# Performance work log

Hardware: AMD Instinct MI355X
Metric: run time of the kernel (lower is better)

The kernel has to match this reference:

```python
import jax, jax.numpy as jnp
import numpy as np

T, B, H, L = 512, 64, 512, 2  # seq len, batch, hidden (=input_size), num_layers


def setup_inputs() -> dict:
    key = jax.random.key(0)
    ks = jax.random.split(key, 8)
    s = 1.0 / np.sqrt(H)  # PyTorch LSTMCell init scale
    return {
        "x": jax.random.normal(ks[0], (T, B, H), dtype=jnp.float32),
        "hx": jax.random.normal(ks[1], (L, B, H), dtype=jnp.float32),
        "cx": jax.random.normal(ks[2], (L, B, H), dtype=jnp.float32),
        "W_ih": jax.random.uniform(ks[3], (L, 4 * H, H), jnp.float32, -s, s),
        "W_hh": jax.random.uniform(ks[4], (L, 4 * H, H), jnp.float32, -s, s),
        "b_ih": jax.random.uniform(ks[5], (L, 4 * H), jnp.float32, -s, s),
        "b_hh": jax.random.uniform(ks[6], (L, 4 * H), jnp.float32, -s, s),
    }


def _lstm_cell(x, h, c, W_ih, W_hh, b_ih, b_hh):
    # gates: [B, 4H], PyTorch gate order i, f, g, o
    gates = x @ W_ih.T + b_ih + h @ W_hh.T + b_hh
    i, f, g, o = jnp.split(gates, 4, axis=-1)
    c_new = jax.nn.sigmoid(f) * c + jax.nn.sigmoid(i) * jnp.tanh(g)
    h_new = jax.nn.sigmoid(o) * jnp.tanh(c_new)
    return h_new, c_new


def reference(x, hx, cx, W_ih, W_hh, b_ih, b_hh):
    num_layers = W_ih.shape[0]

    def step(carry, x_t):
        hs, cs = carry  # each [L, B, H]
        inp = x_t
        new_h, new_c = [], []
        for l in range(num_layers):
            h, c = _lstm_cell(inp, hs[l], cs[l], W_ih[l], W_hh[l], b_ih[l], b_hh[l])
            new_h.append(h)
            new_c.append(c)
            inp = h  # feed current-timestep output to next layer (matches torch code)
        return (jnp.stack(new_h), jnp.stack(new_c)), inp

    (hx_f, cx_f), output = jax.lax.scan(step, (hx, cx), x)
    return output, (hx_f, cx_f)
```

## Files before the change

kernel.cpp:

```cpp
#include <hip/hip_runtime.h>
#include <hip/hip_bf16.h>
#include <stdint.h>

#define Tn 512
#define Bn 64
#define Hn 512
#define LDP 520
#define NWG 128
#define NTHR 512
#define BnHn (Bn * Hn)

typedef unsigned short u16;
typedef unsigned int u32;
typedef unsigned long long u64;
typedef __attribute__((ext_vector_type(8))) short bf16x8;
typedef __attribute__((ext_vector_type(4))) float f32x4;

#define GO_OFF   2048
#define HIST_OFF 16384

__device__ __forceinline__ u16 f2bf(float f) {
  u32 u = __float_as_uint(f);
  u = (u + 0x7FFFu + ((u >> 16) & 1u)) >> 16;
  return (u16)u;
}
__device__ __forceinline__ float sigf(float x) { return 1.f / (1.f + __expf(-x)); }
__device__ __forceinline__ float mytanh(float x) {
  float e = __expf(2.f * x);
  return 1.f - 2.f / (e + 1.f);
}

extern "C" __global__ void __launch_bounds__(256)
lstm_prep(const float* __restrict__ x, const float* __restrict__ hx,
          u32* __restrict__ ws, int xok, int histok) {
  u16* hist = (u16*)((char*)ws + HIST_OFF);
  u16* xbf  = hist + (size_t)(histok ? 513 : 2) * 2 * BnHn;
  const int slot_init = histok ? 512 : 1;
  const int gt = blockIdx.x * 256 + threadIdx.x;
  if (xok) {
#pragma unroll
    for (int i = 0; i < 8; ++i) {
      const int c = gt + (i << 19);
      const float4 v = *(const float4*)(x + (size_t)c * 4);
      const u64 pk = (u64)((u32)f2bf(v.x) | ((u32)f2bf(v.y) << 16)) |
                     ((u64)((u32)f2bf(v.z) | ((u32)f2bf(v.w) << 16)) << 32);
      *(u64*)(xbf + (size_t)c * 4) = pk;
    }
  }
  if (gt < 32768) {
    const int e0 = 2 * gt;
    const int l = e0 >> 15;
    const int off = e0 & 32767;
    const u32 pk = (u32)f2bf(hx[e0]) | ((u32)f2bf(hx[e0 + 1]) << 16);
    *(u32*)(hist + ((size_t)slot_init * 2 + l) * BnHn + off) = pk;
  }
}

extern "C" __global__ void __launch_bounds__(NTHR, 2)
lstm_fused(const float* __restrict__ x, const float* __restrict__ hx,
           const float* __restrict__ cx, const float* __restrict__ Wih,
           const float* __restrict__ Whh, const float* __restrict__ bih,
           const float* __restrict__ bhh, float* __restrict__ out,
           u32* __restrict__ ws, int xok, int histok) {
  __shared__ u16 sh_inp[32 * LDP];
  __shared__ u16 sh_h[32 * LDP];
  __shared__ u32 sh_flag;

  __builtin_amdgcn_fence(__ATOMIC_ACQUIRE, "agent");

  const int wg = blockIdx.x;
  const int tid = threadIdx.x;
  const int layer = wg >> 6;
  const int rem = wg & 63;
  const int shalf = rem >> 5;
  const int cc = rem & 31;
  const int wave = tid >> 6;
  const int lane = tid & 63;
  const int l15 = lane & 15;
  const int lhi = lane >> 4;
  const int mt = wave >> 1;
  const int nt = wave & 1;
  const bool leader_wg = (layer == 0) && (cc == 0);

  u32* slots = ws;
  u32* gof   = ws + GO_OFF;
  u16* hist  = (u16*)((char*)ws + HIST_OFF);
  u16* xbf   = hist + (size_t)(histok ? 513 : 2) * 2 * BnHn;

  if (tid == 0) sh_flag = 0;

  const int jrow = mt * 16 + l15;
  const int gateA = jrow & 3, colA = jrow >> 2;
  const int growA = gateA * Hn + cc * 16 + colA;
  const float* wihp = Wih + ((size_t)layer * 4 * Hn + growA) * Hn;
  const float* whhp = Whh + ((size_t)layer * 4 * Hn + growA) * Hn;
  bf16x8 wih_f[16], whh_f[16];
#pragma unroll
  for (int kt = 0; kt < 16; ++kt) {
    const int k0 = kt * 32 + lhi * 8;
    const float4 va0 = *(const float4*)(wihp + k0);
    const float4 va1 = *(const float4*)(wihp + k0 + 4);
    const float4 vb0 = *(const float4*)(whhp + k0);
    const float4 vb1 = *(const float4*)(whhp + k0 + 4);
    bf16x8 a, b;
    a[0]=(short)f2bf(va0.x); a[1]=(short)f2bf(va0.y); a[2]=(short)f2bf(va0.z); a[3]=(short)f2bf(va0.w);
    a[4]=(short)f2bf(va1.x); a[5]=(short)f2bf(va1.y); a[6]=(short)f2bf(va1.z); a[7]=(short)f2bf(va1.w);
    b[0]=(short)f2bf(vb0.x); b[1]=(short)f2bf(vb0.y); b[2]=(short)f2bf(vb0.z); b[3]=(short)f2bf(vb0.w);
    b[4]=(short)f2bf(vb1.x); b[5]=(short)f2bf(vb1.y); b[6]=(short)f2bf(vb1.z); b[7]=(short)f2bf(vb1.w);
    wih_f[kt] = a; whh_f[kt] = b;
  }

  const int colE = cc * 16 + mt * 4 + lhi;
  const int sampE = shalf * 32 + nt * 16 + l15;
  float bias[4];
#pragma unroll
  for (int r = 0; r < 4; ++r) {
    const int grow = r * Hn + cc * 16 + mt * 4 + lhi;
    bias[r] = bih[layer * 4 * Hn + grow] + bhh[layer * 4 * Hn + grow];
  }
  float c_cur = cx[((size_t)layer * Bn + sampE) * Hn + colE];

  auto stage_x = [&](int t) {
    if (xok) {
      const u16* ip = xbf + ((size_t)t * Bn + shalf * 32) * Hn;
#pragma unroll
      for (int i = 0; i < 4; ++i) {
        const int chunk = tid + i * 512;
        const int row = chunk >> 6, c0 = (chunk & 63) * 8;
        const uint4 v = *(const uint4*)(ip + (size_t)row * Hn + c0);
        *(uint4*)(&sh_inp[row * LDP + c0]) = v;
      }
    } else {
      const float* xp = x + ((size_t)t * Bn + shalf * 32) * Hn;
#pragma unroll
      for (int i = 0; i < 8; ++i) {
        const int chunk = tid + i * 512;
        const int row = chunk >> 7, c0 = (chunk & 127) * 4;
        const float4 v = *(const float4*)(xp + (size_t)row * Hn + c0);
        const u32 p0 = (u32)f2bf(v.x) | ((u32)f2bf(v.y) << 16);
        const u32 p1 = (u32)f2bf(v.z) | ((u32)f2bf(v.w) << 16);
        *(uint2*)(&sh_inp[row * LDP + c0]) = make_uint2(p0, p1);
      }
    }
  };
  if (layer == 0) stage_x(0);

  u32 ep = 0;
  for (int s = 0; s <= Tn; ++s) {
    const int t = layer ? s - 1 : s;
    const bool act = (t >= 0) && (t < Tn);

    if (act) {
      const int slotR = histok ? ((t == 0) ? 512 : (t - 1)) : ((t - 1) & 1);
      const u16* hp = hist + ((size_t)slotR * 2 + layer) * BnHn + (size_t)(shalf * 32) * Hn;
      if (histok) {
#pragma unroll
        for (int i = 0; i < 4; ++i) {
          const int chunk = tid + i * 512;
          const int row = chunk >> 6, c0 = (chunk & 63) * 8;
          const uint4 v = *(const uint4*)(hp + (size_t)row * Hn + c0);
          *(uint4*)(&sh_h[row * LDP + c0]) = v;
        }
      } else {
#pragma unroll
        for (int i = 0; i < 8; ++i) {
          const int chunk = tid + i * 512;
          const int row = chunk >> 7, c0 = (chunk & 127) * 4;
          const u64 v = __hip_atomic_load((const u64*)(hp + (size_t)row * Hn + c0),
                                          __ATOMIC_RELAXED, __HIP_MEMORY_SCOPE_AGENT);
          *(u64*)(&sh_h[row * LDP + c0]) = v;
        }
      }
      if (layer == 1) {
        const int slotI = histok ? t : (t & 1);
        const u16* ip = hist + ((size_t)slotI * 2 + 0) * BnHn + (size_t)(shalf * 32) * Hn;
        if (histok) {
#pragma unroll
          for (int i = 0; i < 4; ++i) {
            const int chunk = tid + i * 512;
            const int row = chunk >> 6, c0 = (chunk & 63) * 8;
            const uint4 v = *(const uint4*)(ip + (size_t)row * Hn + c0);
            *(uint4*)(&sh_inp[row * LDP + c0]) = v;
          }
        } else {
#pragma unroll
          for (int i = 0; i < 8; ++i) {
            const int chunk = tid + i * 512;
            const int row = chunk >> 7, c0 = (chunk & 127) * 4;
            const u64 v = __hip_atomic_load((const u64*)(ip + (size_t)row * Hn + c0),
                                            __ATOMIC_RELAXED, __HIP_MEMORY_SCOPE_AGENT);
            *(u64*)(&sh_inp[row * LDP + c0]) = v;
          }
        }
      }
    }
    __syncthreads();

    float hn = 0.f, cn = 0.f;
    if (act) {
      f32x4 a0 = {0,0,0,0}, a1 = {0,0,0,0}, b0 = {0,0,0,0}, b1 = {0,0,0,0};
      const int brow = (nt * 16 + l15) * LDP;
#pragma unroll
      for (int kt = 0; kt < 16; kt += 2) {
        const bf16x8 bi0 = *(const bf16x8*)(&sh_inp[brow + kt * 32 + lhi * 8]);
        const bf16x8 bh0 = *(const bf16x8*)(&sh_h[brow + kt * 32 + lhi * 8]);
        const bf16x8 bi1 = *(const bf16x8*)(&sh_inp[brow + (kt + 1) * 32 + lhi * 8]);
        const bf16x8 bh1 = *(const bf16x8*)(&sh_h[brow + (kt + 1) * 32 + lhi * 8]);
        a0 = __builtin_amdgcn_mfma_f32_16x16x32_bf16(wih_f[kt], bi0, a0, 0, 0, 0);
        b0 = __builtin_amdgcn_mfma_f32_16x16x32_bf16(whh_f[kt], bh0, b0, 0, 0, 0);
        a1 = __builtin_amdgcn_mfma_f32_16x16x32_bf16(wih_f[kt + 1], bi1, a1, 0, 0, 0);
        b1 = __builtin_amdgcn_mfma_f32_16x16x32_bf16(whh_f[kt + 1], bh1, b1, 0, 0, 0);
      }
      const float gi = a0[0] + a1[0] + b0[0] + b1[0] + bias[0];
      const float gf = a0[1] + a1[1] + b0[1] + b1[1] + bias[1];
      const float gg = a0[2] + a1[2] + b0[2] + b1[2] + bias[2];
      const float go_ = a0[3] + a1[3] + b0[3] + b1[3] + bias[3];
      cn = sigf(gf) * c_cur + sigf(gi) * mytanh(gg);
      hn = sigf(go_) * mytanh(cn);
      c_cur = cn;

      const u32 hu = (u32)f2bf(hn);
      const u32 pair = hu | (__shfl_xor(hu, 16) << 16);
      const u32 hi2 = __shfl_xor(pair, 32);
      if (lhi == 0) {
        const int slotW = histok ? t : (t & 1);
        const u64 v8 = (u64)pair | ((u64)hi2 << 32);
        u16* wp = hist + ((size_t)slotW * 2 + layer) * BnHn + (size_t)sampE * Hn + cc * 16 + mt * 4;
        __hip_atomic_store((u64*)wp, v8, __ATOMIC_RELAXED, __HIP_MEMORY_SCOPE_AGENT);
      }
    }
    asm volatile("s_waitcnt vmcnt(0)" ::: "memory");
    __syncthreads();
    ++ep;
    if (tid == 0)
      __hip_atomic_store(&slots[wg * 16], ep, __ATOMIC_RELAXED, __HIP_MEMORY_SCOPE_AGENT);

    if (act) {
      if (layer == 1)
        out[((size_t)t * Bn + sampE) * Hn + colE] = hn;
      if (t == Tn - 1) {
        out[(size_t)Tn * Bn * Hn + ((size_t)layer * Bn + sampE) * Hn + colE] = hn;
        out[(size_t)Tn * Bn * Hn + (size_t)2 * Bn * Hn + ((size_t)layer * Bn + sampE) * Hn + colE] = cn;
      }
    }
    if (layer == 0 && (s + 1) < Tn) stage_x(s + 1);

    if (s == Tn) break;

    if (wave == 0) {
      if (leader_wg) {
        const int pid = (lane < 32) ? (shalf * 32 + lane)
                                    : (64 + shalf * 32 + (lane - 32));
        const u32* pl = &slots[pid * 16];
        while (true) {
          const u32 v = __hip_atomic_load(pl, __ATOMIC_RELAXED, __HIP_MEMORY_SCOPE_AGENT);
          if (__all((int)(v >= ep))) break;
        }
        __hip_atomic_store(&gof[pid * 16], ep, __ATOMIC_RELAXED, __HIP_MEMORY_SCOPE_AGENT);
      } else {
        while (__hip_atomic_load(&gof[wg * 16], __ATOMIC_RELAXED,
                                 __HIP_MEMORY_SCOPE_AGENT) < ep) {}
      }
      __hip_atomic_store(&sh_flag, ep, __ATOMIC_RELAXED, __HIP_MEMORY_SCOPE_WORKGROUP);
    } else {
      while (__hip_atomic_load(&sh_flag, __ATOMIC_RELAXED, __HIP_MEMORY_SCOPE_WORKGROUP) < ep) {}
    }
    asm volatile("" ::: "memory");
  }
}

extern "C" void kernel_launch(void* const* d_in, const int* in_sizes, int n_in,
                              void* d_out, int out_size, void* d_ws, size_t ws_size,
                              hipStream_t stream) {
  const float* x   = (const float*)d_in[0];
  const float* hx  = (const float*)d_in[1];
  const float* cx  = (const float*)d_in[2];
  const float* Wih = (const float*)d_in[3];
  const float* Whh = (const float*)d_in[4];
  const float* bih = (const float*)d_in[5];
  const float* bhh = (const float*)d_in[6];
  float* outp = (float*)d_out;
  u32* wsp = (u32*)d_ws;

  const size_t slot_bytes = (size_t)2 * Bn * Hn * 2;
  const size_t hist_bytes = (size_t)513 * slot_bytes;
  int histok = (ws_size >= HIST_OFF + hist_bytes) ? 1 : 0;
  const size_t xoff = HIST_OFF + (size_t)(histok ? 513 : 2) * slot_bytes;
  int xok = (ws_size >= xoff + (size_t)Tn * Bn * Hn * 2) ? 1 : 0;

  hipMemsetAsync(d_ws, 0, HIST_OFF, stream);

  lstm_prep<<<dim3(2048), dim3(256), 0, stream>>>(x, hx, wsp, xok, histok);

  void* args[] = {(void*)&x, (void*)&hx, (void*)&cx, (void*)&Wih, (void*)&Whh,
                  (void*)&bih, (void*)&bhh, (void*)&outp, (void*)&wsp,
                  (void*)&xok, (void*)&histok};
  hipError_t e = hipLaunchCooperativeKernel((const void*)lstm_fused, dim3(NWG),
                                            dim3(NTHR), args, 0, stream);
  if (e != hipSuccess) {
    lstm_fused<<<dim3(NWG), dim3(NTHR), 0, stream>>>(x, hx, cx, Wih, Whh, bih, bhh,
                                                     outp, wsp, xok, histok);
  }
}
```

Before: 2.102 ms.

## Replace centralized leader barrier with point-to-point dependency polling and two-step layer lag

Measured after the change: 1.928 ms. 1.09x faster.

```diff
diff --git a/kernel.cpp b/kernel.cpp
--- a/kernel.cpp
+++ b/kernel.cpp
@@ -16,7 +16,6 @@
 typedef __attribute__((ext_vector_type(8))) short bf16x8;
 typedef __attribute__((ext_vector_type(4))) float f32x4;
 
-#define GO_OFF   2048
 #define HIST_OFF 16384
 
 __device__ __forceinline__ u16 f2bf(float f) {
@@ -29,13 +28,16 @@
   float e = __expf(2.f * x);
   return 1.f - 2.f / (e + 1.f);
 }
+__device__ __forceinline__ u32 ald32(const u32* p) {
+  return __hip_atomic_load(p, __ATOMIC_RELAXED, __HIP_MEMORY_SCOPE_AGENT);
+}
 
 extern "C" __global__ void __launch_bounds__(256)
 lstm_prep(const float* __restrict__ x, const float* __restrict__ hx,
           u32* __restrict__ ws, int xok, int histok) {
   u16* hist = (u16*)((char*)ws + HIST_OFF);
-  u16* xbf  = hist + (size_t)(histok ? 513 : 2) * 2 * BnHn;
-  const int slot_init = histok ? 512 : 1;
+  u16* xbf  = hist + (size_t)(histok ? 513 : 4) * 2 * BnHn;
+  const int slot_init = histok ? 512 : 3;
   const int gt = blockIdx.x * 256 + threadIdx.x;
   if (xok) {
 #pragma unroll
@@ -64,7 +66,6 @@
            u32* __restrict__ ws, int xok, int histok) {
   __shared__ u16 sh_inp[32 * LDP];
   __shared__ u16 sh_h[32 * LDP];
-  __shared__ u32 sh_flag;
 
   __builtin_amdgcn_fence(__ATOMIC_ACQUIRE, "agent");
 
@@ -80,14 +81,11 @@
   const int lhi = lane >> 4;
   const int mt = wave >> 1;
   const int nt = wave & 1;
-  const bool leader_wg = (layer == 0) && (cc == 0);
 
   u32* slots = ws;
-  u32* gof   = ws + GO_OFF;
   u16* hist  = (u16*)((char*)ws + HIST_OFF);
-  u16* xbf   = hist + (size_t)(histok ? 513 : 2) * 2 * BnHn;
-
-  if (tid == 0) sh_flag = 0;
+  u16* xbf   = hist + (size_t)(histok ? 513 : 4) * 2 * BnHn;
+  const int init_slot = histok ? 512 : 3;
 
   const int jrow = mt * 16 + l15;
   const int gateA = jrow & 3, colA = jrow >> 2;
@@ -120,6 +118,17 @@
   }
   float c_cur = cx[((size_t)layer * Bn + sampE) * Hn + colE];
 
+  int pid, tgtoff;
+  if (layer == 0) {
+    if (lane < 32) { pid = shalf * 32 + lane; tgtoff = 0; }
+    else if (histok) { pid = shalf * 32 + (lane - 32); tgtoff = 0; }
+    else { pid = 64 + shalf * 32 + (lane - 32); tgtoff = 1; }
+  } else {
+    if (lane < 32) { pid = 64 + shalf * 32 + lane; tgtoff = 0; }
+    else { pid = shalf * 32 + (lane - 32); tgtoff = 1; }
+  }
+  const u32* pollp = &slots[pid * 16];
+
   auto stage_x = [&](int t) {
     if (xok) {
       const u16* ip = xbf + ((size_t)t * Bn + shalf * 32) * Hn;
@@ -143,55 +152,41 @@
       }
     }
   };
+  auto stage_h = [&](int slot, int srclayer, u16* dst) {
+    const u16* hp = hist + ((size_t)slot * 2 + srclayer) * BnHn + (size_t)(shalf * 32) * Hn;
+    if (histok) {
+#pragma unroll
+      for (int i = 0; i < 4; ++i) {
+        const int chunk = tid + i * 512;
+        const int row = chunk >> 6, c0 = (chunk & 63) * 8;
+        const uint4 v = *(const uint4*)(hp + (size_t)row * Hn + c0);
+        *(uint4*)(&dst[row * LDP + c0]) = v;
+      }
+    } else {
+#pragma unroll
+      for (int i = 0; i < 8; ++i) {
+        const int chunk = tid + i * 512;
+        const int row = chunk >> 7, c0 = (chunk & 127) * 4;
+        const u64 v = __hip_atomic_load((const u64*)(hp + (size_t)row * Hn + c0),
+                                        __ATOMIC_RELAXED, __HIP_MEMORY_SCOPE_AGENT);
+        *(u64*)(&dst[row * LDP + c0]) = v;
+      }
+    }
+  };
   if (layer == 0) stage_x(0);
 
+  const int smax = Tn + 1;
   u32 ep = 0;
-  for (int s = 0; s <= Tn; ++s) {
-    const int t = layer ? s - 1 : s;
+  for (int s = 0; s <= smax; ++s) {
+    const int t = layer ? s - 2 : s;
     const bool act = (t >= 0) && (t < Tn);
 
     if (act) {
-      const int slotR = histok ? ((t == 0) ? 512 : (t - 1)) : ((t - 1) & 1);
-      const u16* hp = hist + ((size_t)slotR * 2 + layer) * BnHn + (size_t)(shalf * 32) * Hn;
-      if (histok) {
-#pragma unroll
-        for (int i = 0; i < 4; ++i) {
-          const int chunk = tid + i * 512;
-          const int row = chunk >> 6, c0 = (chunk & 63) * 8;
-          const uint4 v = *(const uint4*)(hp + (size_t)row * Hn + c0);
-          *(uint4*)(&sh_h[row * LDP + c0]) = v;
-        }
-      } else {
-#pragma unroll
-        for (int i = 0; i < 8; ++i) {
-          const int chunk = tid + i * 512;
-          const int row = chunk >> 7, c0 = (chunk & 127) * 4;
-          const u64 v = __hip_atomic_load((const u64*)(hp + (size_t)row * Hn + c0),
-                                          __ATOMIC_RELAXED, __HIP_MEMORY_SCOPE_AGENT);
-          *(u64*)(&sh_h[row * LDP + c0]) = v;
-        }
-      }
+      const int slotR = (t == 0) ? init_slot : (histok ? (t - 1) : ((t - 1) & 3));
+      stage_h(slotR, layer, sh_h);
       if (layer == 1) {
-        const int slotI = histok ? t : (t & 1);
-        const u16* ip = hist + ((size_t)slotI * 2 + 0) * BnHn + (size_t)(shalf * 32) * Hn;
-        if (histok) {
-#pragma unroll
-          for (int i = 0; i < 4; ++i) {
-            const int chunk = tid + i * 512;
-            const int row = chunk >> 6, c0 = (chunk & 63) * 8;
-            const uint4 v = *(const uint4*)(ip + (size_t)row * Hn + c0);
-            *(uint4*)(&sh_inp[row * LDP + c0]) = v;
-          }
-        } else {
-#pragma unroll
-          for (int i = 0; i < 8; ++i) {
-            const int chunk = tid + i * 512;
-            const int row = chunk >> 7, c0 = (chunk & 127) * 4;
-            const u64 v = __hip_atomic_load((const u64*)(ip + (size_t)row * Hn + c0),
-                                            __ATOMIC_RELAXED, __HIP_MEMORY_SCOPE_AGENT);
-            *(u64*)(&sh_inp[row * LDP + c0]) = v;
-          }
-        }
+        const int slotI = histok ? t : (t & 3);
+        stage_h(slotI, 0, sh_inp);
       }
     }
     __syncthreads();
@@ -223,7 +218,7 @@
       const u32 pair = hu | (__shfl_xor(hu, 16) << 16);
       const u32 hi2 = __shfl_xor(pair, 32);
       if (lhi == 0) {
-        const int slotW = histok ? t : (t & 1);
+        const int slotW = histok ? t : (t & 3);
         const u64 v8 = (u64)pair | ((u64)hi2 << 32);
         u16* wp = hist + ((size_t)slotW * 2 + layer) * BnHn + (size_t)sampE * Hn + cc * 16 + mt * 4;
         __hip_atomic_store((u64*)wp, v8, __ATOMIC_RELAXED, __HIP_MEMORY_SCOPE_AGENT);
@@ -245,26 +240,15 @@
     }
     if (layer == 0 && (s + 1) < Tn) stage_x(s + 1);
 
-    if (s == Tn) break;
+    if (s == smax) break;
 
     if (wave == 0) {
-      if (leader_wg) {
-        const int pid = (lane < 32) ? (shalf * 32 + lane)
-                                    : (64 + shalf * 32 + (lane - 32));
-        const u32* pl = &slots[pid * 16];
-        while (true) {
-          const u32 v = __hip_atomic_load(pl, __ATOMIC_RELAXED, __HIP_MEMORY_SCOPE_AGENT);
-          if (__all((int)(v >= ep))) break;
-        }
-        __hip_atomic_store(&gof[pid * 16], ep, __ATOMIC_RELAXED, __HIP_MEMORY_SCOPE_AGENT);
-      } else {
-        while (__hip_atomic_load(&gof[wg * 16], __ATOMIC_RELAXED,
-                                 __HIP_MEMORY_SCOPE_AGENT) < ep) {}
-      }
-      __hip_atomic_store(&sh_flag, ep, __ATOMIC_RELAXED, __HIP_MEMORY_SCOPE_WORKGROUP);
-    } else {
-      while (__hip_atomic_load(&sh_flag, __ATOMIC_RELAXED, __HIP_MEMORY_SCOPE_WORKGROUP) < ep) {}
-    }
+      while (true) {
+        const u32 v = ald32(pollp);
+        if (__all((int)(v + (u32)tgtoff >= ep))) break;
+      }
+    }
+    __syncthreads();
     asm volatile("" ::: "memory");
   }
 }
@@ -283,9 +267,8 @@
   u32* wsp = (u32*)d_ws;
 
   const size_t slot_bytes = (size_t)2 * Bn * Hn * 2;
-  const size_t hist_bytes = (size_t)513 * slot_bytes;
-  int histok = (ws_size >= HIST_OFF + hist_bytes) ? 1 : 0;
-  const size_t xoff = HIST_OFF + (size_t)(histok ? 513 : 2) * slot_bytes;
+  int histok = (ws_size >= HIST_OFF + (size_t)513 * slot_bytes) ? 1 : 0;
+  const size_t xoff = HIST_OFF + (size_t)(histok ? 513 : 4) * slot_bytes;
   int xok = (ws_size >= xoff + (size_t)Tn * Bn * Hn * 2) ? 1 : 0;
 
   hipMemsetAsync(d_ws, 0, HIST_OFF, stream);
```
